# Kernel tuning notes

Measured on AMD Instinct MI355X. Metric: run time of the kernel, lower is better.

Reference implementation:

```python
import jax, jax.numpy as jnp
import numpy as np

B, T, IN, H, NH = 64, 512, 1024, 1024, 4
HD = H // NH  # head_dim = 256
NG = 3        # gates: z (update), r (reset), n (candidate)


def setup_inputs() -> dict:
    key = jax.random.key(0)
    k1, k2, k3, k4, k5 = jax.random.split(key, 5)
    inp = jax.random.normal(k1, (B, T, IN), dtype=jnp.float32)
    # nn.Linear(input_size, 3*hidden_size): weight [3H, IN], bias [3H]
    W = jax.random.normal(k2, (IN, NG * H), dtype=jnp.float32) / np.sqrt(IN)
    bW = jax.random.normal(k3, (NG * H,), dtype=jnp.float32) * 0.02
    # recurrent R: [num_heads, head_dim_in, num_gates, head_dim_out], std=1/sqrt(head_dim)
    R = jax.random.normal(k4, (NH, HD, NG, HD), dtype=jnp.float32) / np.sqrt(HD)
    b = jax.random.normal(k5, (NH, NG, HD), dtype=jnp.float32)
    return {"input": inp, "W": W, "bW": bW, "R": R, "b": b}


def _gru_scan(Wx, R, b, h0):
    # Wx: [T, B, NH, NG, HD], h0: [B, NH, HD]
    def step(h, wx):
        # recurrent gate preactivations: Ry[b,h,g,o] = sum_i h[b,h,i] R[h,i,g,o]
        ry = jnp.einsum('bhi,higo->bhgo', h, R)
        z = jax.nn.sigmoid(wx[:, :, 0] + ry[:, :, 0] + b[:, 0])
        r = jax.nn.sigmoid(wx[:, :, 1] + ry[:, :, 1] + b[:, 1])
        n = jnp.tanh(wx[:, :, 2] + r * ry[:, :, 2] + b[:, 2])
        h_new = z * h + (1.0 - z) * n
        return h_new, h_new

    h_last, hs = jax.lax.scan(step, h0, Wx)
    return hs, h_last  # hs: [T, B, NH, HD]


def reference(input, W, bW, R, b):
    bs, sl = input.shape[0], input.shape[1]
    # input projection for all timesteps at once
    Wx = input @ W + bW                               # [B, T, NG*H]
    Wx = Wx.reshape(bs, sl, NG, NH, HD)
    Wx = jnp.transpose(Wx, (1, 0, 3, 2, 4))           # [T, B, NH, NG, HD]
    h0 = jnp.zeros((bs, NH, HD), dtype=input.dtype)
    hs, h_last = _gru_scan(Wx, R, b, h0)
    h = jnp.transpose(hs, (1, 0, 2, 3)).reshape(bs, sl, H)   # [B, T, H]
    hn = h_last.reshape(1, bs, H)                             # [num_layers=1, B, H]
    return h, hn
```

## Files before the change

### kernel.cpp

```cpp
#include <hip/hip_runtime.h>
#include <hip/hip_fp16.h>


typedef _Float16 f16x8 __attribute__((ext_vector_type(8)));
typedef float    f32x4 __attribute__((ext_vector_type(4)));

#define AS1 __attribute__((address_space(1)))
#define AS3 __attribute__((address_space(3)))

__device__ __forceinline__ void async_ld16(const void* g, void* l) {
    __builtin_amdgcn_global_load_lds((const AS1 void*)g, (AS3 void*)l, 16, 0, 0);
}

#if defined(__has_builtin)
#if __has_builtin(__builtin_amdgcn_rcpf)
#define RCPF(x) __builtin_amdgcn_rcpf(x)
#endif
#endif
#ifndef RCPF
#define RCPF(x) (1.f / (x))
#endif

__device__ __forceinline__ float sigmoidf_(float x) {
    return RCPF(1.f + __expf(-x));
}
__device__ __forceinline__ float tanhf_(float x) {
    float e = __expf(-2.f * fabsf(x));
    float r = (1.f - e) * RCPF(1.f + e);
    return copysignf(r, x);
}

__global__ __launch_bounds__(256) void cast_to_f16(const float* __restrict__ in,
                                                   _Float16* __restrict__ out, int n8) {
    int i = blockIdx.x * 256 + threadIdx.x;
    if (i >= n8) return;
    const float4* p = (const float4*)in;
    float4 a = p[2 * i], b = p[2 * i + 1];
    f16x8 r;
    r[0] = (_Float16)a.x; r[1] = (_Float16)a.y; r[2] = (_Float16)a.z; r[3] = (_Float16)a.w;
    r[4] = (_Float16)b.x; r[5] = (_Float16)b.y; r[6] = (_Float16)b.z; r[7] = (_Float16)b.w;
    *(f16x8*)(out + (size_t)i * 8) = r;
}

__global__ __launch_bounds__(256) void transpose_cast(const float* __restrict__ W,
                                                      _Float16* __restrict__ WT) {
    __shared__ float tile[32][33];
    const int tx = threadIdx.x, ty = threadIdx.y;
    const int n0 = blockIdx.x * 32, k0 = blockIdx.y * 32;
#pragma unroll
    for (int j = 0; j < 32; j += 8)
        tile[ty + j][tx] = W[(size_t)(k0 + ty + j) * 3072 + n0 + tx];
    __syncthreads();
#pragma unroll
    for (int j = 0; j < 32; j += 8)
        WT[(size_t)(n0 + ty + j) * 1024 + k0 + tx] = (_Float16)tile[tx][ty + j];
}

__global__ __launch_bounds__(256) void gemm_wx(const _Float16* __restrict__ A,
                                               const _Float16* __restrict__ BT,
                                               const float* __restrict__ bW,
                                               const float* __restrict__ bR,
                                               float* __restrict__ Wx) {
    __shared__ _Float16 As[128 * 32];
    __shared__ _Float16 Bs[128 * 32];
    const int tid  = threadIdx.x;
    const int wave = tid >> 6, lane = tid & 63;
    const int m0 = blockIdx.y * 128, n0 = blockIdx.x * 128;
    const int wm = (wave >> 1) * 64, wn = (wave & 1) * 64;
    const int r16 = lane & 15, kq = lane >> 4;

    f32x4 acc[4][4];
#pragma unroll
    for (int m = 0; m < 4; m++)
#pragma unroll
        for (int n = 0; n < 4; n++) acc[m][n] = (f32x4){0.f, 0.f, 0.f, 0.f};

    const int srow = wave * 32 + (lane >> 2);
    const int scol = (lane & 3) * 8;

    for (int kt = 0; kt < 32; kt++) {
        const int k0 = kt * 32;
#pragma unroll
        for (int j = 0; j < 2; j++) {
            async_ld16(A  + (size_t)(m0 + srow + j * 16) * 1024 + k0 + scol,
                       As + (wave * 32 + j * 16) * 32);
            async_ld16(BT + (size_t)(n0 + srow + j * 16) * 1024 + k0 + scol,
                       Bs + (wave * 32 + j * 16) * 32);
        }
        __syncthreads();
        f16x8 af[4], bf[4];
#pragma unroll
        for (int m = 0; m < 4; m++) af[m] = *(const f16x8*)(As + (wm + m * 16 + r16) * 32 + kq * 8);
#pragma unroll
        for (int n = 0; n < 4; n++) bf[n] = *(const f16x8*)(Bs + (wn + n * 16 + r16) * 32 + kq * 8);
#pragma unroll
        for (int m = 0; m < 4; m++)
#pragma unroll
            for (int n = 0; n < 4; n++)
                acc[m][n] = __builtin_amdgcn_mfma_f32_16x16x32_f16(af[m], bf[n], acc[m][n], 0, 0, 0);
        __syncthreads();
    }

#pragma unroll
    for (int m = 0; m < 4; m++) {
        const int row0 = m0 + wm + m * 16 + (lane >> 4) * 4;
#pragma unroll
        for (int n = 0; n < 4; n++) {
            const int col  = n0 + wn + n * 16 + r16;
            const int g    = col >> 10, head = (col >> 8) & 3, o = col & 255;
            const float bias = bW[col] + bR[head * 768 + g * 256 + o];
#pragma unroll
            for (int q = 0; q < 4; q++) {
                const int rr = row0 + q;
                const int t = rr & 511, bb = rr >> 9;
                Wx[(((size_t)t * 64 + bb) * 12 + head * 3 + g) * 256 + o] = acc[m][n][q] + bias;
            }
        }
    }
}

__global__ __launch_bounds__(512) void scan_mfma(const float* __restrict__ R,
                                                 const float* __restrict__ Wx,
                                                 float* __restrict__ out) {
    __shared__ _Float16 Rbuf[3 * 256 * 40];
    __shared__ _Float16 h16[2 * 256];

    const int bx = blockIdx.x;
    const int head = bx >> 6, b = bx & 63;
    const int t0 = threadIdx.x;
    const int w = t0 >> 6, l = t0 & 63;
    const int c = l & 15, kq = l >> 4;
    const int o0 = w * 32;

    f16x8 Bf[3][2][7];
#pragma unroll
    for (int kt = 0; kt < 8; kt++) {
        __syncthreads();
        for (int idx = t0; idx < 32 * 768; idx += 512) {
            const int ii = idx / 768;
            const int rem = idx - ii * 768;
            const int g = rem >> 8, o = rem & 255;
            Rbuf[(g * 256 + o) * 40 + ii] =
                (_Float16)R[(((size_t)head * 256 + kt * 32 + ii) * 3 + g) * 256 + o];
        }
        __syncthreads();
        if (kt < 7) {
#pragma unroll
            for (int g = 0; g < 3; g++)
#pragma unroll
                for (int ot = 0; ot < 2; ot++)
                    Bf[g][ot][kt] =
                        *(const f16x8*)(Rbuf + ((size_t)(g * 256 + o0 + ot * 16 + c)) * 40 + kq * 8);
        }
    }

    h16[t0] = (_Float16)0.f;

    float hprev[2] = {0.f, 0.f};
    float* outb = out + ((size_t)b * 512) * 1024 + head * 256;
    float* hnp  = out + (size_t)64 * 512 * 1024 + b * 1024 + head * 256;

    float wxc[3][2];
#pragma unroll
    for (int g = 0; g < 3; g++)
#pragma unroll
        for (int o2 = 0; o2 < 2; o2++)
            wxc[g][o2] = Wx[(((size_t)0 * 64 + b) * 12 + head * 3 + g) * 256 + o0 + o2 * 16 + c];
    __syncthreads();

    int cur = 0;
    for (int t = 0; t < 512; t++) {
        const _Float16* hc = h16 + cur * 256;

        if (t > 0 && kq == 0) {
#pragma unroll
            for (int o2 = 0; o2 < 2; o2++)
                outb[(size_t)(t - 1) * 1024 + o0 + o2 * 16 + c] = hprev[o2];
        }
        float wxn[3][2];
        if (t < 511) {
#pragma unroll
            for (int g = 0; g < 3; g++)
#pragma unroll
                for (int o2 = 0; o2 < 2; o2++)
                    wxn[g][o2] = Wx[(((size_t)(t + 1) * 64 + b) * 12 + head * 3 + g) * 256 +
                                    o0 + o2 * 16 + c];
        } else {
            wxn[0][0] = wxn[0][1] = wxn[1][0] = wxn[1][1] = wxn[2][0] = wxn[2][1] = 0.f;
        }

        f16x8 Bs7[3][2];
#pragma unroll
        for (int g = 0; g < 3; g++)
#pragma unroll
            for (int ot = 0; ot < 2; ot++)
                Bs7[g][ot] =
                    *(const f16x8*)(Rbuf + ((size_t)(g * 256 + o0 + ot * 16 + c)) * 40 + kq * 8);
        f16x8 Af0 = *(const f16x8*)(hc + 0 * 32 + kq * 8);

        f32x4 acc[3][2];
#pragma unroll
        for (int g = 0; g < 3; g++)
#pragma unroll
            for (int ot = 0; ot < 2; ot++) acc[g][ot] = (f32x4){0.f, 0.f, 0.f, 0.f};

#pragma unroll
        for (int kt = 0; kt < 8; kt++) {
            f16x8 Af1;
            if (kt < 7) Af1 = *(const f16x8*)(hc + (kt + 1) * 32 + kq * 8);
#pragma unroll
            for (int g = 0; g < 3; g++)
#pragma unroll
                for (int ot = 0; ot < 2; ot++)
                    acc[g][ot] = __builtin_amdgcn_mfma_f32_16x16x32_f16(
                        Af0, (kt < 7) ? Bf[g][ot][kt] : Bs7[g][ot], acc[g][ot], 0, 0, 0);
            Af0 = Af1;
        }

        _Float16* hw = h16 + (cur ^ 1) * 256;
#pragma unroll
        for (int o2 = 0; o2 < 2; o2++) {
            const float z = sigmoidf_(wxc[0][o2] + acc[0][o2][0]);
            const float r = sigmoidf_(wxc[1][o2] + acc[1][o2][0]);
            const float n = tanhf_(wxc[2][o2] + r * acc[2][o2][0]);
            const float h = n + z * (hprev[o2] - n);
            hprev[o2] = h;
            if (kq == 0) hw[o0 + o2 * 16 + c] = (_Float16)h;
        }
#pragma unroll
        for (int g = 0; g < 3; g++)
#pragma unroll
            for (int o2 = 0; o2 < 2; o2++) wxc[g][o2] = wxn[g][o2];

        __syncthreads();
        cur ^= 1;
    }
    if (kq == 0) {
#pragma unroll
        for (int o2 = 0; o2 < 2; o2++) {
            outb[(size_t)511 * 1024 + o0 + o2 * 16 + c] = hprev[o2];
            hnp[o0 + o2 * 16 + c] = hprev[o2];
        }
    }
}

extern "C" void kernel_launch(void* const* d_in, const int* in_sizes, int n_in,
                              void* d_out, int out_size, void* d_ws, size_t ws_size,
                              hipStream_t stream) {
    (void)in_sizes; (void)n_in; (void)out_size; (void)ws_size;
    const float* inp = (const float*)d_in[0];
    const float* W   = (const float*)d_in[1];
    const float* bW  = (const float*)d_in[2];
    const float* R   = (const float*)d_in[3];
    const float* bR  = (const float*)d_in[4];
    float* out = (float*)d_out;

    _Float16* A16 = (_Float16*)d_ws;
    _Float16* WT  = (_Float16*)((char*)d_ws + 67108864);
    float*    Wx  = (float*)((char*)d_ws + 73400320);

    cast_to_f16<<<16384, 256, 0, stream>>>(inp, A16, 4194304);
    transpose_cast<<<dim3(96, 32), dim3(32, 8), 0, stream>>>(W, WT);
    gemm_wx<<<dim3(24, 256), 256, 0, stream>>>(A16, WT, bW, bR, Wx);
    scan_mfma<<<256, 512, 0, stream>>>(R, Wx, out);
}
```

Measured before the change: 993.9 us.

## Store Wx projection in fp16 and keep all R fragments in registers

The GEMM now writes the input projection as fp16 instead of fp32, halving both the Wx write traffic and the per-step reads in the scan. The scan holds all eight k-slices of R in registers, which removes the per-step LDS reload of the last slice, and it stages R into LDS with vectorized 8-element stores. The cost is lower precision in the gate preactivations and higher register pressure in the 512-thread scan kernel, which could cause spills.

After: 1.019 ms. +2.5%, slower.

```diff
diff --git a/kernel.cpp b/kernel.cpp
--- a/kernel.cpp
+++ b/kernel.cpp
@@ -60,7 +60,7 @@
                                                const _Float16* __restrict__ BT,
                                                const float* __restrict__ bW,
                                                const float* __restrict__ bR,
-                                               float* __restrict__ Wx) {
+                                               _Float16* __restrict__ Wx) {
     __shared__ _Float16 As[128 * 32];
     __shared__ _Float16 Bs[128 * 32];
     const int tid  = threadIdx.x;
@@ -113,14 +113,15 @@
             for (int q = 0; q < 4; q++) {
                 const int rr = row0 + q;
                 const int t = rr & 511, bb = rr >> 9;
-                Wx[(((size_t)t * 64 + bb) * 12 + head * 3 + g) * 256 + o] = acc[m][n][q] + bias;
+                Wx[(((size_t)t * 64 + bb) * 12 + head * 3 + g) * 256 + o] =
+                    (_Float16)(acc[m][n][q] + bias);
             }
         }
     }
 }
 
 __global__ __launch_bounds__(512) void scan_mfma(const float* __restrict__ R,
-                                                 const float* __restrict__ Wx,
+                                                 const _Float16* __restrict__ Wx,
                                                  float* __restrict__ out) {
     __shared__ _Float16 Rbuf[3 * 256 * 40];
     __shared__ _Float16 h16[2 * 256];
@@ -132,26 +133,27 @@
     const int c = l & 15, kq = l >> 4;
     const int o0 = w * 32;
 
-    f16x8 Bf[3][2][7];
+    f16x8 Bf[3][2][8];
 #pragma unroll
     for (int kt = 0; kt < 8; kt++) {
         __syncthreads();
-        for (int idx = t0; idx < 32 * 768; idx += 512) {
-            const int ii = idx / 768;
-            const int rem = idx - ii * 768;
+        for (int item = t0; item < 3072; item += 512) {
+            const int q = item / 768;
+            const int rem = item - q * 768;
             const int g = rem >> 8, o = rem & 255;
-            Rbuf[(g * 256 + o) * 40 + ii] =
-                (_Float16)R[(((size_t)head * 256 + kt * 32 + ii) * 3 + g) * 256 + o];
-        }
-        __syncthreads();
-        if (kt < 7) {
-#pragma unroll
-            for (int g = 0; g < 3; g++)
-#pragma unroll
-                for (int ot = 0; ot < 2; ot++)
-                    Bf[g][ot][kt] =
-                        *(const f16x8*)(Rbuf + ((size_t)(g * 256 + o0 + ot * 16 + c)) * 40 + kq * 8);
-        }
+            const float* rp = R + (((size_t)head * 256 + kt * 32 + q * 8) * 3 + g) * 256 + o;
+            f16x8 v;
+#pragma unroll
+            for (int j = 0; j < 8; j++) v[j] = (_Float16)rp[(size_t)j * 768];
+            *(f16x8*)(Rbuf + ((size_t)(g * 256 + o)) * 40 + q * 8) = v;
+        }
+        __syncthreads();
+#pragma unroll
+        for (int g = 0; g < 3; g++)
+#pragma unroll
+            for (int ot = 0; ot < 2; ot++)
+                Bf[g][ot][kt] =
+                    *(const f16x8*)(Rbuf + ((size_t)(g * 256 + o0 + ot * 16 + c)) * 40 + kq * 8);
     }
 
     h16[t0] = (_Float16)0.f;
@@ -160,12 +162,13 @@
     float* outb = out + ((size_t)b * 512) * 1024 + head * 256;
     float* hnp  = out + (size_t)64 * 512 * 1024 + b * 1024 + head * 256;
 
+    const _Float16* wxbase = Wx + ((size_t)b * 12 + head * 3) * 256;
     float wxc[3][2];
 #pragma unroll
     for (int g = 0; g < 3; g++)
 #pragma unroll
         for (int o2 = 0; o2 < 2; o2++)
-            wxc[g][o2] = Wx[(((size_t)0 * 64 + b) * 12 + head * 3 + g) * 256 + o0 + o2 * 16 + c];
+            wxc[g][o2] = (float)wxbase[g * 256 + o0 + o2 * 16 + c];
     __syncthreads();
 
     int cur = 0;
@@ -179,31 +182,23 @@
         }
         float wxn[3][2];
         if (t < 511) {
+            const _Float16* wp = wxbase + (size_t)(t + 1) * 196608;
 #pragma unroll
             for (int g = 0; g < 3; g++)
 #pragma unroll
                 for (int o2 = 0; o2 < 2; o2++)
-                    wxn[g][o2] = Wx[(((size_t)(t + 1) * 64 + b) * 12 + head * 3 + g) * 256 +
-                                    o0 + o2 * 16 + c];
+                    wxn[g][o2] = (float)wp[g * 256 + o0 + o2 * 16 + c];
         } else {
             wxn[0][0] = wxn[0][1] = wxn[1][0] = wxn[1][1] = wxn[2][0] = wxn[2][1] = 0.f;
         }
 
-        f16x8 Bs7[3][2];
+        f32x4 acc[3][2];
 #pragma unroll
         for (int g = 0; g < 3; g++)
 #pragma unroll
-            for (int ot = 0; ot < 2; ot++)
-                Bs7[g][ot] =
-                    *(const f16x8*)(Rbuf + ((size_t)(g * 256 + o0 + ot * 16 + c)) * 40 + kq * 8);
+            for (int ot = 0; ot < 2; ot++) acc[g][ot] = (f32x4){0.f, 0.f, 0.f, 0.f};
+
         f16x8 Af0 = *(const f16x8*)(hc + 0 * 32 + kq * 8);
-
-        f32x4 acc[3][2];
-#pragma unroll
-        for (int g = 0; g < 3; g++)
-#pragma unroll
-            for (int ot = 0; ot < 2; ot++) acc[g][ot] = (f32x4){0.f, 0.f, 0.f, 0.f};
-
 #pragma unroll
         for (int kt = 0; kt < 8; kt++) {
             f16x8 Af1;
@@ -213,7 +208,7 @@
 #pragma unroll
                 for (int ot = 0; ot < 2; ot++)
                     acc[g][ot] = __builtin_amdgcn_mfma_f32_16x16x32_f16(
-                        Af0, (kt < 7) ? Bf[g][ot][kt] : Bs7[g][ot], acc[g][ot], 0, 0, 0);
+                        Af0, Bf[g][ot][kt], acc[g][ot], 0, 0, 0);
             Af0 = Af1;
         }
 
@@ -257,7 +252,7 @@
 
     _Float16* A16 = (_Float16*)d_ws;
     _Float16* WT  = (_Float16*)((char*)d_ws + 67108864);
-    float*    Wx  = (float*)((char*)d_ws + 73400320);
+    _Float16* Wx  = (_Float16*)((char*)d_ws + 73400320);
 
     cast_to_f16<<<16384, 256, 0, stream>>>(inp, A16, 4194304);
     transpose_cast<<<dim3(96, 32), dim3(32, 8), 0, stream>>>(W, WT);
```
